# Performance work log

Measured on AMD Instinct MI355X. Metric: run time of the kernel, lower is better.

Reference implementation:

```python
import jax, jax.numpy as jnp
import numpy as np

B, S, D = 2, 2048, 1024
H, KV, HD = 16, 4, 64          # heads, kv heads, head_dim = D//H
I, E, K = 3584, 4, 2            # ffn intermediate, routed experts, top_k
WIN = 512                       # sliding window
EPS = 1e-5
THETA = 1000000.0
LIMIT = 7.0                     # swiglu clamp
NREP = H // KV
NEG = -1e30

def _rms(x, w):
    return x * jax.lax.rsqrt(jnp.mean(x * x, axis=-1, keepdims=True) + EPS) * w

def _rot_half(x):
    h = x.shape[-1] // 2
    return jnp.concatenate([-x[..., h:], x[..., :h]], axis=-1)

def _ffn(x, gw, uw, dw):
    g = jnp.minimum(x @ gw.T, LIMIT)
    u = jnp.clip(x @ uw.T, -LIMIT, LIMIT)
    return (jax.nn.silu(g) * u) @ dw.T

def setup_inputs():
    key = jax.random.key(0)
    ks = jax.random.split(key, 16)
    # rotary embeddings [S, HD]
    inv = 1.0 / (THETA ** (jnp.arange(0, HD, 2, dtype=jnp.float32) / HD))
    freqs = jnp.outer(jnp.arange(S, dtype=jnp.float32), inv)
    emb = jnp.concatenate([freqs, freqs], axis=-1)
    s = 0.02
    return dict(
        x=jax.random.normal(ks[0], (B, S, D), jnp.float32),
        cos=jnp.cos(emb), sin=jnp.sin(emb),
        attn_norm_w=jnp.ones((D,), jnp.float32),
        post_norm_w=jnp.ones((D,), jnp.float32),
        q_norm_w=jnp.ones((HD,), jnp.float32),
        k_norm_w=jnp.ones((HD,), jnp.float32),
        wq=jax.random.normal(ks[1], (H * HD, D), jnp.float32) * s,
        wk=jax.random.normal(ks[2], (KV * HD, D), jnp.float32) * s,
        wv=jax.random.normal(ks[3], (KV * HD, D), jnp.float32) * s,
        wo=jax.random.normal(ks[4], (D, H * HD), jnp.float32) * s,
        sinks=jax.random.normal(ks[5], (H,), jnp.float32),
        gate_w=jax.random.normal(ks[6], (E, D), jnp.float32) * s,
        eg_w=jax.random.normal(ks[7], (E, I, D), jnp.float32) * s,
        eu_w=jax.random.normal(ks[8], (E, I, D), jnp.float32) * s,
        ed_w=jax.random.normal(ks[9], (E, D, I), jnp.float32) * s,
        sg_w=jax.random.normal(ks[10], (I, D), jnp.float32) * s,
        su_w=jax.random.normal(ks[11], (I, D), jnp.float32) * s,
        sd_w=jax.random.normal(ks[12], (D, I), jnp.float32) * s,
    )

def _forward(x, cos, sin, attn_norm_w, wq, wk, wv, wo, q_norm_w, k_norm_w,
             sinks, post_norm_w, gate_w, eg_w, eu_w, ed_w, sg_w, su_w, sd_w):
    # ---- attention sublayer ----
    hin = _rms(x, attn_norm_w)
    q = (hin @ wq.T).reshape(B, S, H, HD)
    k = (hin @ wk.T).reshape(B, S, KV, HD)
    v = (hin @ wv.T).reshape(B, S, KV, HD)
    q = _rms(q, q_norm_w)
    k = _rms(k, k_norm_w)
    c, sn = cos[None, :, None, :], sin[None, :, None, :]
    q = q * c + _rot_half(q) * sn
    k = k * c + _rot_half(k) * sn
    k = jnp.repeat(k, NREP, axis=2)  # GQA -> [B,S,H,HD]
    v = jnp.repeat(v, NREP, axis=2)
    scores = jnp.einsum('bihd,bjhd->bhij', q, k) / np.sqrt(HD).astype(np.float32)
    idx = jnp.arange(S)
    allowed = (idx[:, None] >= idx[None, :]) & (idx[None, :] > idx[:, None] - WIN)
    scores = jnp.where(allowed[None, None], scores, NEG)
    sink = jnp.broadcast_to(sinks.reshape(1, H, 1, 1), (B, H, S, 1))
    ext = jnp.concatenate([scores, sink], axis=-1)           # [B,H,S,S+1]
    w = jax.nn.softmax(ext.astype(jnp.float32), axis=-1)[..., :-1].astype(x.dtype)
    attn = jnp.einsum('bhij,bjhd->bihd', w, v).reshape(B, S, H * HD) @ wo.T
    h1 = x + attn
    # ---- MoE FFN sublayer ----
    m = _rms(h1, post_norm_w).reshape(-1, D)                 # [T,D]
    T = m.shape[0]
    gs = jax.nn.softmax(m @ gate_w.T, axis=-1)               # [T,E]
    tw, ti = jax.lax.top_k(gs, K)
    tw = tw / (jnp.sum(tw, axis=-1, keepdims=True) + 1e-20)  # norm_topk_prob
    wd = jnp.zeros((T, E), m.dtype).at[jnp.arange(T)[:, None], ti].add(tw)
    g = jnp.minimum(jnp.einsum('td,eid->tei', m, eg_w), LIMIT)
    u = jnp.clip(jnp.einsum('td,eid->tei', m, eu_w), -LIMIT, LIMIT)
    eo = jnp.einsum('tei,edi->ted', jax.nn.silu(g) * u, ed_w)
    y = jnp.einsum('ted,te->td', eo, wd) + _ffn(m, sg_w, su_w, sd_w)
    return h1 + y.reshape(B, S, D)

def reference(x, cos, sin, attn_norm_w, post_norm_w, q_norm_w, k_norm_w,
              wq, wk, wv, wo, sinks, gate_w, eg_w, eu_w, ed_w, sg_w, su_w, sd_w):
    return _forward(x, cos, sin, attn_norm_w, wq, wk, wv, wo, q_norm_w, k_norm_w,
                    sinks, post_norm_w, gate_w, eg_w, eu_w, ed_w, sg_w, su_w, sd_w)
```

## Files before the change

### kernel.cpp

```cpp
#include <hip/hip_runtime.h>
#include <cstdint>
#include <cstddef>

#define S_LEN 2048
#define BATCH 2
#define DMODEL 1024
#define NH 16
#define NKV 4
#define HDIM 64
#define NTOK 4096
#define IDIM 3584
#define NEXP 4
#define WINSZ 512
#define EPSV 1e-5f
#define LIMV 7.0f
#define CATMAX 13056

typedef unsigned short u16;
typedef unsigned int u32;
typedef __bf16 bf16x8 __attribute__((ext_vector_type(8)));
typedef float f32x4 __attribute__((ext_vector_type(4)));
typedef u32 u32x4 __attribute__((ext_vector_type(4)));
typedef u16 u16x4 __attribute__((ext_vector_type(4)));

__device__ __forceinline__ u16 f2b(float f) {
  union { float f; u32 u; } v; v.f = f;
  return (u16)((v.u + 0x7fffu + ((v.u >> 16) & 1u)) >> 16);
}
__device__ __forceinline__ float b2f(u16 h) {
  union { u32 u; float f; } v; v.u = ((u32)h) << 16; return v.f;
}
__device__ __forceinline__ float wave_sum(float x) {
#pragma unroll
  for (int o = 32; o > 0; o >>= 1) x += __shfl_xor(x, o);
  return x;
}
__device__ __forceinline__ void gld16(const void* g, void* l) {
  __builtin_amdgcn_global_load_lds(
      (const __attribute__((address_space(1))) u32*)g,
      (__attribute__((address_space(3))) u32*)l, 16, 0, 0);
}

__global__ void k_init(int* cnt) {
  if (threadIdx.x < NEXP) cnt[threadIdx.x] = 0;
}

struct CvtArgs {
  const float* src[10];
  u16* dh[10];
  u16* dl[10];
  int n4[10];
};
__global__ __launch_bounds__(256) void k_convert(CvtArgs a) {
  int ai = blockIdx.y;
  const f32x4* s = (const f32x4*)a.src[ai];
  u16* dh = a.dh[ai];
  u16* dl = a.dl[ai];
  int n4 = a.n4[ai];
  for (int i = blockIdx.x * 256 + threadIdx.x; i < n4; i += gridDim.x * 256) {
    f32x4 v = s[i];
    u16x4 h;
    h.x = f2b(v.x); h.y = f2b(v.y); h.z = f2b(v.z); h.w = f2b(v.w);
    ((u16x4*)dh)[i] = h;
    if (dl) {
      u16x4 lo;
      lo.x = f2b(v.x - b2f(h.x)); lo.y = f2b(v.y - b2f(h.y));
      lo.z = f2b(v.z - b2f(h.z)); lo.w = f2b(v.w - b2f(h.w));
      ((u16x4*)dl)[i] = lo;
    }
  }
}

__global__ __launch_bounds__(256) void k_rms_split(const float* __restrict__ x,
                                                   const float* __restrict__ w,
                                                   u16* __restrict__ oh, u16* __restrict__ ol) {
  int row = blockIdx.x;
  int t = threadIdx.x;
  const f32x4* xr = (const f32x4*)(x + (size_t)row * DMODEL);
  f32x4 v = xr[t];
  float ss = v.x * v.x + v.y * v.y + v.z * v.z + v.w * v.w;
  ss = wave_sum(ss);
  __shared__ float red[4];
  int wid = t >> 6;
  if ((t & 63) == 0) red[wid] = ss;
  __syncthreads();
  float tot = red[0] + red[1] + red[2] + red[3];
  float r = rsqrtf(tot * (1.0f / DMODEL) + EPSV);
  f32x4 wv = ((const f32x4*)w)[t];
  float y0 = v.x * r * wv.x, y1 = v.y * r * wv.y, y2 = v.z * r * wv.z, y3 = v.w * r * wv.w;
  u16x4 h; h.x = f2b(y0); h.y = f2b(y1); h.z = f2b(y2); h.w = f2b(y3);
  u16x4 lo; lo.x = f2b(y0 - b2f(h.x)); lo.y = f2b(y1 - b2f(h.y));
  lo.z = f2b(y2 - b2f(h.z)); lo.w = f2b(y3 - b2f(h.w));
  ((u16x4*)(oh + (size_t)row * DMODEL))[t] = h;
  ((u16x4*)(ol + (size_t)row * DMODEL))[t] = lo;
}

__global__ __launch_bounds__(256) void k_qkprep(const float* __restrict__ qkv,
                                                const float* __restrict__ cosb,
                                                const float* __restrict__ sinb,
                                                const float* __restrict__ qw,
                                                const float* __restrict__ kw,
                                                u16* __restrict__ qhh, u16* __restrict__ qll,
                                                u16* __restrict__ khh, u16* __restrict__ kll,
                                                u16* __restrict__ vhh, u16* __restrict__ vll) {
  int t = blockIdx.x;
  int b = t / S_LEN, s = t - b * S_LEN;
  int wid = threadIdx.x >> 6, l = threadIdx.x & 63;
  const float* row = qkv + (size_t)t * 1536;
  float c = cosb[s * 64 + l], sn = sinb[s * 64 + l];
#pragma unroll
  for (int ii = 0; ii < 6; ii++) {
    int u = wid + 4 * ii;
    if (u < 16) {
      float v = row[u * 64 + l];
      float ss = wave_sum(v * v);
      float r = rsqrtf(ss * (1.0f / 64.0f) + EPSV);
      float vn = v * r * qw[l];
      float p = __shfl_xor(vn, 32);
      float o = (l < 32) ? (vn * c - p * sn) : (vn * c + p * sn);
      o *= 0.125f;
      size_t base = (((size_t)(b * NH + u)) * S_LEN + s) * 64 + l;
      u16 hi = f2b(o);
      qhh[base] = hi; qll[base] = f2b(o - b2f(hi));
    } else if (u < 20) {
      int kv = u - 16;
      float v = row[1024 + kv * 64 + l];
      float ss = wave_sum(v * v);
      float r = rsqrtf(ss * (1.0f / 64.0f) + EPSV);
      float vn = v * r * kw[l];
      float p = __shfl_xor(vn, 32);
      float o = (l < 32) ? (vn * c - p * sn) : (vn * c + p * sn);
      size_t base = (((size_t)(b * NKV + kv)) * S_LEN + s) * 64 + l;
      u16 hi = f2b(o);
      khh[base] = hi; kll[base] = f2b(o - b2f(hi));
    } else {
      int kv = u - 20;
      float v = row[1280 + kv * 64 + l];
      size_t base = (((size_t)(b * NKV + kv)) * S_LEN + s) * 64 + l;
      u16 hi = f2b(v);
      vhh[base] = hi; vll[base] = f2b(v - b2f(hi));
    }
  }
}

__global__ __launch_bounds__(256) void k_vtrans(const u16* __restrict__ vh,
                                                const u16* __restrict__ vl,
                                                u16* __restrict__ vth, u16* __restrict__ vtl) {
  int kb = blockIdx.x;
  int gg = blockIdx.y;
  __shared__ u16 Th[128 * 64], Tl[128 * 64];
  int t = threadIdx.x;
  const u16* sh = vh + (((size_t)gg * S_LEN) + kb * 128) * 64;
  const u16* sl = vl + (((size_t)gg * S_LEN) + kb * 128) * 64;
#pragma unroll
  for (int p = 0; p < 8; p++) {
    int idx = p * 256 + t;
    int key = idx >> 4, dq = idx & 15;
    u16x4 a = *(const u16x4*)(sh + key * 64 + dq * 4);
    u16x4 bb = *(const u16x4*)(sl + key * 64 + dq * 4);
    int off = key * 128 + ((dq * 8) ^ ((key & 7) << 4));
    *(u16x4*)((char*)Th + off) = a;
    *(u16x4*)((char*)Tl + off) = bb;
  }
  __syncthreads();
  int d = t >> 2, kq = t & 3;
  u16 outh[32], outl[32];
#pragma unroll
  for (int jj = 0; jj < 32; jj++) {
    int key = kq * 32 + jj;
    int off = key * 128 + ((d * 2) ^ ((key & 7) << 4));
    outh[jj] = *(const u16*)((const char*)Th + off);
    outl[jj] = *(const u16*)((const char*)Tl + off);
  }
  u16* dsth = vth + (((size_t)gg * 64) + d) * S_LEN + kb * 128 + kq * 32;
  u16* dstl = vtl + (((size_t)gg * 64) + d) * S_LEN + kb * 128 + kq * 32;
#pragma unroll
  for (int q4 = 0; q4 < 8; q4++) {
    u16x4 a = {outh[q4 * 4], outh[q4 * 4 + 1], outh[q4 * 4 + 2], outh[q4 * 4 + 3]};
    u16x4 bb = {outl[q4 * 4], outl[q4 * 4 + 1], outl[q4 * 4 + 2], outl[q4 * 4 + 3]};
    *(u16x4*)(dsth + q4 * 4) = a;
    *(u16x4*)(dstl + q4 * 4) = bb;
  }
}

__global__ __launch_bounds__(256) void k_attn_mfma(
    const u16* __restrict__ qhp, const u16* __restrict__ qlp,
    const u16* __restrict__ khp, const u16* __restrict__ klp,
    const u16* __restrict__ vthp, const u16* __restrict__ vtlp,
    const float* __restrict__ sinks,
    u16* __restrict__ oh, u16* __restrict__ ol) {
  int qt = blockIdx.x;
  int bh = blockIdx.y;
  int h = bh & 15, b = bh >> 4;
  int kvg = b * NKV + (h >> 2);
  int qbase = qt * 64;
  int t = threadIdx.x, w = t >> 6, l = t & 63;
  int g = l >> 4, li = l & 15;

  __shared__ u16 Qh[4096], Ql[4096], Kh[4096], Kl[4096], Vh[4096], Vl[4096];
  __shared__ u16 Ph[4][1024], Pl[4][1024];

  {
    const u16* sh = qhp + (((size_t)bh * S_LEN) + qbase) * 64;
    const u16* sl = qlp + (((size_t)bh * S_LEN) + qbase) * 64;
#pragma unroll
    for (int p = 0; p < 2; p++) {
      int idx = p * 256 + t;
      int row = idx >> 3, seg = idx & 7;
      u32x4 a = *(const u32x4*)(sh + row * 64 + seg * 8);
      u32x4 bb = *(const u32x4*)(sl + row * 64 + seg * 8);
      int off = row * 128 + ((seg * 16) ^ ((row & 7) << 4));
      *(u32x4*)((char*)Qh + off) = a;
      *(u32x4*)((char*)Ql + off) = bb;
    }
  }

  float m_[4], lsum[4];
  f32x4 accv[4];
  float sk = sinks[h];
#pragma unroll
  for (int j = 0; j < 4; j++) { m_[j] = sk; lsum[j] = 1.0f; }
#pragma unroll
  for (int nt = 0; nt < 4; nt++) accv[nt] = (f32x4){0.f, 0.f, 0.f, 0.f};

  int j0s = qbase - WINSZ; if (j0s < 0) j0s = 0;
  const u16* khb = khp + ((size_t)kvg * S_LEN) * 64;
  const u16* klb = klp + ((size_t)kvg * S_LEN) * 64;
  const u16* vthb = vthp + ((size_t)kvg * 64) * S_LEN;
  const u16* vtlb = vtlp + ((size_t)kvg * 64) * S_LEN;

  for (int j0 = j0s; j0 <= qbase; j0 += 64) {
    __syncthreads();
#pragma unroll
    for (int p = 0; p < 2; p++) {
      int idx = p * 256 + t;
      int row = idx >> 3, seg = idx & 7;
      int off = row * 128 + ((seg * 16) ^ ((row & 7) << 4));
      *(u32x4*)((char*)Kh + off) = *(const u32x4*)(khb + ((size_t)(j0 + row)) * 64 + seg * 8);
      *(u32x4*)((char*)Kl + off) = *(const u32x4*)(klb + ((size_t)(j0 + row)) * 64 + seg * 8);
      *(u32x4*)((char*)Vh + off) = *(const u32x4*)(vthb + (size_t)row * S_LEN + j0 + seg * 8);
      *(u32x4*)((char*)Vl + off) = *(const u32x4*)(vtlb + (size_t)row * S_LEN + j0 + seg * 8);
    }
    __syncthreads();

    f32x4 S[4];
#pragma unroll
    for (int nt = 0; nt < 4; nt++) S[nt] = (f32x4){0.f, 0.f, 0.f, 0.f};
#pragma unroll
    for (int ks = 0; ks < 2; ks++) {
      int arow = w * 16 + li;
      int coff = ks * 64 + g * 16;
      int ao = arow * 128 + (coff ^ ((arow & 7) << 4));
      bf16x8 qah = *(const bf16x8*)((char*)Qh + ao);
      bf16x8 qal = *(const bf16x8*)((char*)Ql + ao);
#pragma unroll
      for (int nt = 0; nt < 4; nt++) {
        int brow = nt * 16 + li;
        int bo = brow * 128 + (coff ^ ((brow & 7) << 4));
        bf16x8 kbh = *(const bf16x8*)((char*)Kh + bo);
        bf16x8 kbl = *(const bf16x8*)((char*)Kl + bo);
        S[nt] = __builtin_amdgcn_mfma_f32_16x16x32_bf16(qah, kbh, S[nt], 0, 0, 0);
        S[nt] = __builtin_amdgcn_mfma_f32_16x16x32_bf16(qah, kbl, S[nt], 0, 0, 0);
        S[nt] = __builtin_amdgcn_mfma_f32_16x16x32_bf16(qal, kbh, S[nt], 0, 0, 0);
      }
    }

    float scj[4];
#pragma unroll
    for (int j = 0; j < 4; j++) {
      int q = qbase + w * 16 + g * 4 + j;
      float sv[4];
      float mx = -1e30f;
#pragma unroll
      for (int nt = 0; nt < 4; nt++) {
        int key = j0 + nt * 16 + li;
        bool ok = (key <= q) && (key > q - WINSZ);
        sv[nt] = ok ? S[nt][j] : -1e30f;
        mx = fmaxf(mx, sv[nt]);
      }
#pragma unroll
      for (int o = 1; o < 16; o <<= 1) mx = fmaxf(mx, __shfl_xor(mx, o));
      float mn = fmaxf(m_[j], mx);
      float sc = __expf(m_[j] - mn);
      float ps = 0.f;
      float pv[4];
#pragma unroll
      for (int nt = 0; nt < 4; nt++) { pv[nt] = __expf(sv[nt] - mn); ps += pv[nt]; }
#pragma unroll
      for (int o = 1; o < 16; o <<= 1) ps += __shfl_xor(ps, o);
      lsum[j] = lsum[j] * sc + ps;
      m_[j] = mn;
      scj[j] = sc;
      int prow = g * 4 + j;
#pragma unroll
      for (int nt = 0; nt < 4; nt++) {
        int pb = prow * 128 + ((nt * 32 + li * 2) ^ ((prow & 7) << 4));
        u16 hi = f2b(pv[nt]);
        *(u16*)((char*)Ph[w] + pb) = hi;
        *(u16*)((char*)Pl[w] + pb) = f2b(pv[nt] - b2f(hi));
      }
    }
#pragma unroll
    for (int nt = 0; nt < 4; nt++) {
      f32x4 a = accv[nt];
      a[0] *= scj[0]; a[1] *= scj[1]; a[2] *= scj[2]; a[3] *= scj[3];
      accv[nt] = a;
    }

#pragma unroll
    for (int ks = 0; ks < 2; ks++) {
      int coff = ks * 64 + g * 16;
      int pb = li * 128 + (coff ^ ((li & 7) << 4));
      bf16x8 pah = *(const bf16x8*)((char*)Ph[w] + pb);
      bf16x8 pal = *(const bf16x8*)((char*)Pl[w] + pb);
#pragma unroll
      for (int nt = 0; nt < 4; nt++) {
        int vrow = nt * 16 + li;
        int vo = vrow * 128 + (coff ^ ((vrow & 7) << 4));
        bf16x8 vbh = *(const bf16x8*)((char*)Vh + vo);
        bf16x8 vbl = *(const bf16x8*)((char*)Vl + vo);
        accv[nt] = __builtin_amdgcn_mfma_f32_16x16x32_bf16(pah, vbh, accv[nt], 0, 0, 0);
        accv[nt] = __builtin_amdgcn_mfma_f32_16x16x32_bf16(pah, vbl, accv[nt], 0, 0, 0);
        accv[nt] = __builtin_amdgcn_mfma_f32_16x16x32_bf16(pal, vbh, accv[nt], 0, 0, 0);
      }
    }
  }

  float inv[4];
#pragma unroll
  for (int j = 0; j < 4; j++) inv[j] = 1.0f / lsum[j];
#pragma unroll
  for (int nt = 0; nt < 4; nt++) {
#pragma unroll
    for (int j = 0; j < 4; j++) {
      float o = accv[nt][j] * inv[j];
      int token = b * S_LEN + qbase + w * 16 + g * 4 + j;
      size_t off = (size_t)token * (NH * HDIM) + h * 64 + nt * 16 + li;
      u16 hi = f2b(o);
      oh[off] = hi;
      ol[off] = f2b(o - b2f(hi));
    }
  }
}

__global__ __launch_bounds__(256) void k_routing1(const float* __restrict__ h1,
                                                  const float* __restrict__ pw,
                                                  const float* __restrict__ gw,
                                                  u16* __restrict__ mb,
                                                  float* __restrict__ lgbuf) {
  int row = blockIdx.x;
  int t = threadIdx.x;
  int wid = t >> 6;
  const f32x4* xr = (const f32x4*)(h1 + (size_t)row * DMODEL);
  f32x4 v = xr[t];
  float ss = wave_sum(v.x * v.x + v.y * v.y + v.z * v.z + v.w * v.w);
  __shared__ float red[4];
  __shared__ float redp[4][4];
  if ((t & 63) == 0) red[wid] = ss;
  __syncthreads();
  float tot = red[0] + red[1] + red[2] + red[3];
  float r = rsqrtf(tot * (1.0f / DMODEL) + EPSV);
  f32x4 w4 = ((const f32x4*)pw)[t];
  float m0 = v.x * r * w4.x, m1 = v.y * r * w4.y, m2 = v.z * r * w4.z, m3 = v.w * r * w4.w;
  u16x4 hb; hb.x = f2b(m0); hb.y = f2b(m1); hb.z = f2b(m2); hb.w = f2b(m3);
  ((u16x4*)(mb + (size_t)row * DMODEL))[t] = hb;
#pragma unroll
  for (int e = 0; e < NEXP; e++) {
    f32x4 g4 = ((const f32x4*)(gw + (size_t)e * DMODEL))[t];
    float pe = wave_sum(m0 * g4.x + m1 * g4.y + m2 * g4.z + m3 * g4.w);
    if ((t & 63) == 0) redp[wid][e] = pe;
  }
  __syncthreads();
  if (t < NEXP) {
    float lg = redp[0][t] + redp[1][t] + redp[2][t] + redp[3][t];
    lgbuf[(size_t)row * NEXP + t] = lg;
  }
}

__global__ __launch_bounds__(256) void k_route2(const float* __restrict__ lgbuf,
                                                float* __restrict__ wd,
                                                int* __restrict__ cnt,
                                                int* __restrict__ idxb) {
  __shared__ int lcnt[NEXP], gbase[NEXP];
  int t = threadIdx.x;
  int token = blockIdx.x * 256 + t;
  if (t < NEXP) lcnt[t] = 0;
  __syncthreads();
  f32x4 lgv = ((const f32x4*)lgbuf)[token];
  float lg[4] = {lgv.x, lgv.y, lgv.z, lgv.w};
  int i1 = 0;
#pragma unroll
  for (int e = 1; e < NEXP; e++) if (lg[e] > lg[i1]) i1 = e;
  int i2 = -1;
#pragma unroll
  for (int e = 0; e < NEXP; e++) if (e != i1 && (i2 < 0 || lg[e] > lg[i2])) i2 = e;
  float d = __expf(lg[i2] - lg[i1]);
  float w1 = 1.0f / (1.0f + d);
  float w2 = 1.0f - w1;
  float wrow[4] = {0.f, 0.f, 0.f, 0.f};
  wrow[i1] = w1; wrow[i2] = w2;
  ((f32x4*)wd)[token] = (f32x4){wrow[0], wrow[1], wrow[2], wrow[3]};
  int r1 = atomicAdd(&lcnt[i1], 1);
  int r2 = atomicAdd(&lcnt[i2], 1);
  __syncthreads();
  if (t < NEXP) gbase[t] = atomicAdd(&cnt[t], lcnt[t]);
  __syncthreads();
  idxb[i1 * NTOK + gbase[i1] + r1] = token * 2;
  idxb[i2 * NTOK + gbase[i2] + r2] = token * 2 + 1;
}

__global__ __launch_bounds__(256) void k_route3(const int* __restrict__ cnt,
                                                const int* __restrict__ idxb,
                                                const float* __restrict__ wd,
                                                int* __restrict__ idxcat,
                                                float* __restrict__ wcat,
                                                int* __restrict__ pref) {
  int i = blockIdx.x * 256 + threadIdx.x;
  int c0 = cnt[0], c1 = cnt[1], c2 = cnt[2], c3 = cnt[3];
  int p1 = (c0 + 255) & ~255;
  int p2 = p1 + ((c1 + 255) & ~255);
  int p3 = p2 + ((c2 + 255) & ~255);
  int p4 = p3 + ((c3 + 255) & ~255);
  int p5 = p4 + NTOK;
  if (i == 0) {
    pref[0] = 0; pref[1] = p1; pref[2] = p2; pref[3] = p3; pref[4] = p4; pref[5] = p5;
  }
  if (i >= CATMAX) return;
  if (i >= p5) { idxcat[i] = -1; wcat[i] = 0.f; return; }
  if (i >= p4) {
    idxcat[i] = (i - p4) * 4 + 2;
    wcat[i] = 1.0f;
    return;
  }
  int e, base, cn;
  if (i < p1) { e = 0; base = 0; cn = c0; }
  else if (i < p2) { e = 1; base = p1; cn = c1; }
  else if (i < p3) { e = 2; base = p2; cn = c2; }
  else { e = 3; base = p3; cn = c3; }
  int j = i - base;
  if (j < cn) {
    int entry = idxb[e * NTOK + j];
    idxcat[i] = (entry >> 1) * 4 + (entry & 1);
    wcat[i] = wd[(size_t)(entry >> 1) * NEXP + e];
  } else {
    idxcat[i] = -1;
    wcat[i] = 0.f;
  }
}

template <bool DUAL>
__global__ __launch_bounds__(512, 1) void k256(
    const u16* __restrict__ A, const u16* __restrict__ B1e,
    const u16* __restrict__ B2e,
    int lda, int ldb, int K,
    const int* __restrict__ idxcat, const float* __restrict__ wcat,
    const int* __restrict__ pref,
    u16* __restrict__ actout, u16* __restrict__ y3) {
  __shared__ u16 As[4][256 * 32];
  __shared__ u16 B1s[4][128 * 32];
  __shared__ u16 B2s[4][DUAL ? 128 * 32 : 1];
  int tm = blockIdx.y, tn = blockIdx.x;
  int Meff = pref[5];
  int r0 = tm * 256;
  if (r0 >= Meff) return;
  int e = (r0 < pref[1]) ? 0 : (r0 < pref[2]) ? 1 : (r0 < pref[3]) ? 2
          : (r0 < pref[4]) ? 3 : 4;
  const u16* B1 = B1e + (size_t)e * IDIM * DMODEL;
  const u16* B2 = DUAL ? (B2e + (size_t)e * IDIM * DMODEL) : nullptr;

  int t = threadIdx.x;
  int w = t >> 6, l = t & 63;
  int wm = w >> 2, wn = w & 3;
  int li = l & 15, lh = l >> 4;

  size_t aG[2];
#pragma unroll
  for (int c = 0; c < 2; c++) {
    int g = c * 512 + t;
    int rowi = g >> 2, seg = g & 3;
    int srcc = (seg - (rowi >> 2)) & 3;
    int row;
    if constexpr (DUAL) {
      int en = idxcat[r0 + rowi];
      row = (en >= 0) ? (en >> 2) : 0;
    } else {
      row = r0 + rowi;
    }
    aG[c] = (size_t)row * lda + srcc * 8;
  }
  size_t bG;
  {
    int rowi = t >> 2, seg = t & 3;
    int srcc = (seg - (rowi >> 2)) & 3;
    bG = (size_t)(tn * 128 + rowi) * ldb + srcc * 8;
  }
  int wlds = w * 1024;

  int sread = (lh + (li >> 2)) & 3;
  int abase = (wm * 128 + li) * 64 + sread * 16;
  int bbase = (wn * 32 + li) * 64 + sread * 16;

  f32x4 acc[8][2];
  f32x4 accU[DUAL ? 8 : 1][2];
#pragma unroll
  for (int f = 0; f < 8; f++)
#pragma unroll
    for (int cf = 0; cf < 2; cf++) {
      acc[f][cf] = (f32x4){0.f, 0.f, 0.f, 0.f};
      if constexpr (DUAL) accU[f][cf] = (f32x4){0.f, 0.f, 0.f, 0.f};
    }

  auto stage = [&](u16* as, u16* b1s, u16* b2s, int k0) {
    gld16(A + aG[0] + k0, (char*)as + wlds);
    gld16(A + aG[1] + k0, (char*)as + 8192 + wlds);
    gld16(B1 + bG + k0, (char*)b1s + wlds);
    if constexpr (DUAL) gld16(B2 + bG + k0, (char*)b2s + wlds);
  };

  int NT = K >> 5;
  stage(As[0], B1s[0], B2s[0], 0);
  stage(As[1], B1s[1], B2s[1], 32);
  stage(As[2], B1s[2], B2s[2], 64);

  auto iter = [&](int tt, u16* as, u16* b1s, u16* b2s,
                  u16* asN, u16* b1sN, u16* b2sN) {
    if (tt + 3 < NT) stage(asN, b1sN, b2sN, (tt + 3) << 5);
    __builtin_amdgcn_sched_barrier(0);
    if constexpr (DUAL) {
      asm volatile("s_waitcnt vmcnt(12)" ::: "memory");
    } else {
      asm volatile("s_waitcnt vmcnt(9)" ::: "memory");
    }
    __builtin_amdgcn_s_barrier();
    __builtin_amdgcn_sched_barrier(0);
    bf16x8 af[8];
#pragma unroll
    for (int f = 0; f < 8; f++)
      af[f] = *(const bf16x8*)((const char*)as + abase + f * 1024);
    bf16x8 b1f[2];
#pragma unroll
    for (int cf = 0; cf < 2; cf++)
      b1f[cf] = *(const bf16x8*)((const char*)b1s + bbase + cf * 1024);
#pragma unroll
    for (int f = 0; f < 8; f++)
#pragma unroll
      for (int cf = 0; cf < 2; cf++)
        acc[f][cf] = __builtin_amdgcn_mfma_f32_16x16x32_bf16(af[f], b1f[cf], acc[f][cf], 0, 0, 0);
    if constexpr (DUAL) {
      bf16x8 b2f[2];
#pragma unroll
      for (int cf = 0; cf < 2; cf++)
        b2f[cf] = *(const bf16x8*)((const char*)b2s + bbase + cf * 1024);
#pragma unroll
      for (int f = 0; f < 8; f++)
#pragma unroll
        for (int cf = 0; cf < 2; cf++)
          accU[f][cf] = __builtin_amdgcn_mfma_f32_16x16x32_bf16(af[f], b2f[cf], accU[f][cf], 0, 0, 0);
    }
    __builtin_amdgcn_s_barrier();
    __builtin_amdgcn_sched_barrier(0);
  };

  for (int kt = 0; kt < NT; kt += 4) {
    iter(kt + 0, As[0], B1s[0], B2s[0], As[3], B1s[3], B2s[3]);
    iter(kt + 1, As[1], B1s[1], B2s[1], As[0], B1s[0], B2s[0]);
    iter(kt + 2, As[2], B1s[2], B2s[2], As[1], B1s[1], B2s[1]);
    iter(kt + 3, As[3], B1s[3], B2s[3], As[2], B1s[2], B2s[2]);
  }

#pragma unroll
  for (int f = 0; f < 8; f++) {
#pragma unroll
    for (int j = 0; j < 4; j++) {
      int r = r0 + wm * 128 + f * 16 + lh * 4 + j;
#pragma unroll
      for (int cf = 0; cf < 2; cf++) {
        int c = tn * 128 + wn * 32 + cf * 16 + li;
        if constexpr (DUAL) {
          float g = acc[f][cf][j];
          float u = accU[f][cf][j];
          float gm = fminf(g, LIMV);
          float um = fminf(fmaxf(u, -LIMV), LIMV);
          float a = gm / (1.0f + __expf(-gm)) * um;
          actout[(size_t)r * IDIM + c] = f2b(a);
        } else {
          int entry = idxcat[r];
          if (entry >= 0) {
            int tok = entry >> 2, slot = entry & 3;
            y3[((size_t)slot * NTOK + tok) * DMODEL + c] = f2b(wcat[r] * acc[f][cf][j]);
          }
        }
      }
    }
  }
}

constexpr int EPI_STORE = 0;
constexpr int EPI_H1 = 1;

template <int EPI>
__global__ __launch_bounds__(256, 2) void k_gemm(
    const u16* __restrict__ Ah, const u16* __restrict__ Al,
    const u16* __restrict__ Bh, const u16* __restrict__ Bl,
    int M, int N, int K, int lda, int ldb,
    float* __restrict__ outF, int ldc, int col0,
    const float* __restrict__ addsrc) {
  __shared__ u16 As[2 * 128 * 32];
  __shared__ u16 Bs[2 * 128 * 32];
  int tm = blockIdx.y, tn = blockIdx.x;
  int t = threadIdx.x;
  int w = t >> 6, l = t & 63;
  int wr = w >> 1, wc = w & 1;

  size_t a0 = (size_t)(tm * 128 + (t >> 2)) * lda + (t & 3) * 8;
  size_t a1 = a0 + (size_t)64 * lda;
  size_t b0 = (size_t)(tn * 128 + (t >> 2)) * ldb + (t & 3) * 8;
  size_t b1 = b0 + (size_t)64 * ldb;

  char* AsW0 = (char*)As + w * 1024;
  char* AsW1 = (char*)As + 4096 + w * 1024;
  char* BsW0 = (char*)Bs + w * 1024;
  char* BsW1 = (char*)Bs + 4096 + w * 1024;

  f32x4 acc[4][4];
#pragma unroll
  for (int i = 0; i < 4; i++)
#pragma unroll
    for (int j = 0; j < 4; j++) acc[i][j] = (f32x4){0.f, 0.f, 0.f, 0.f};

  int arow = wr * 64 + (l & 15);
  int brow = wc * 64 + (l & 15);
  int koff = (l >> 4) * 8;

  for (int k0 = 0; k0 < K; k0 += 32) {
    __syncthreads();
    gld16(Ah + a0 + k0, AsW0);
    gld16(Ah + a1 + k0, AsW1);
    gld16(Bh + b0 + k0, BsW0);
    gld16(Bh + b1 + k0, BsW1);
    gld16(Al + a0 + k0, AsW0 + 8192);
    gld16(Al + a1 + k0, AsW1 + 8192);
    gld16(Bl + b0 + k0, BsW0 + 8192);
    gld16(Bl + b1 + k0, BsW1 + 8192);
    __syncthreads();
    bf16x8 af[2][4], bf[2][4];
#pragma unroll
    for (int mm = 0; mm < 4; mm++) {
      af[0][mm] = *(const bf16x8*)&As[(arow + mm * 16) * 32 + koff];
      bf[0][mm] = *(const bf16x8*)&Bs[(brow + mm * 16) * 32 + koff];
      af[1][mm] = *(const bf16x8*)&As[128 * 32 + (arow + mm * 16) * 32 + koff];
      bf[1][mm] = *(const bf16x8*)&Bs[128 * 32 + (brow + mm * 16) * 32 + koff];
    }
#pragma unroll
    for (int mi = 0; mi < 4; mi++)
#pragma unroll
      for (int ni = 0; ni < 4; ni++) {
        acc[mi][ni] = __builtin_amdgcn_mfma_f32_16x16x32_bf16(af[0][mi], bf[0][ni], acc[mi][ni], 0, 0, 0);
        acc[mi][ni] = __builtin_amdgcn_mfma_f32_16x16x32_bf16(af[0][mi], bf[1][ni], acc[mi][ni], 0, 0, 0);
        acc[mi][ni] = __builtin_amdgcn_mfma_f32_16x16x32_bf16(af[1][mi], bf[0][ni], acc[mi][ni], 0, 0, 0);
      }
  }

  int rb = tm * 128 + wr * 64 + ((l >> 4) << 2);
  int cb = tn * 128 + wc * 64 + (l & 15);
#pragma unroll
  for (int mi = 0; mi < 4; mi++) {
#pragma unroll
    for (int j = 0; j < 4; j++) {
      int r = rb + mi * 16 + j;
#pragma unroll
      for (int ni = 0; ni < 4; ni++) {
        int c = cb + ni * 16;
        float v = acc[mi][ni][j];
        if constexpr (EPI == EPI_STORE) {
          outF[(size_t)r * ldc + col0 + c] = v;
        } else {
          size_t o = (size_t)r * ldc + c;
          outF[o] = v + addsrc[o];
        }
      }
    }
  }
}

__global__ __launch_bounds__(256) void k_final(const float* __restrict__ h1,
                                               const u16* __restrict__ y3,
                                               float* __restrict__ out) {
  int i = blockIdx.x * 256 + threadIdx.x;
  f32x4 a = ((const f32x4*)h1)[i];
  u16x4 s0 = ((const u16x4*)y3)[i];
  u16x4 s1 = ((const u16x4*)(y3 + (size_t)NTOK * DMODEL))[i];
  u16x4 s2 = ((const u16x4*)(y3 + (size_t)2 * NTOK * DMODEL))[i];
  f32x4 r = {a.x + b2f(s0.x) + b2f(s1.x) + b2f(s2.x),
             a.y + b2f(s0.y) + b2f(s1.y) + b2f(s2.y),
             a.z + b2f(s0.z) + b2f(s1.z) + b2f(s2.z),
             a.w + b2f(s0.w) + b2f(s1.w) + b2f(s2.w)};
  ((f32x4*)out)[i] = r;
}

extern "C" void kernel_launch(void* const* d_in, const int* in_sizes, int n_in,
                              void* d_out, int out_size, void* d_ws, size_t ws_size,
                              hipStream_t stream) {
  (void)in_sizes; (void)n_in; (void)out_size; (void)ws_size;
  const float* x = (const float*)d_in[0];
  const float* cosb = (const float*)d_in[1];
  const float* sinb = (const float*)d_in[2];
  const float* anw = (const float*)d_in[3];
  const float* pnw = (const float*)d_in[4];
  const float* qnw = (const float*)d_in[5];
  const float* knw = (const float*)d_in[6];
  const float* wq = (const float*)d_in[7];
  const float* wk = (const float*)d_in[8];
  const float* wv = (const float*)d_in[9];
  const float* wo = (const float*)d_in[10];
  const float* sinks = (const float*)d_in[11];
  const float* gw = (const float*)d_in[12];
  const float* egw = (const float*)d_in[13];
  const float* euw = (const float*)d_in[14];
  const float* edw = (const float*)d_in[15];
  const float* sgw = (const float*)d_in[16];
  const float* suw = (const float*)d_in[17];
  const float* sdw = (const float*)d_in[18];
  float* out = (float*)d_out;

  char* ws = (char*)d_ws;
  size_t off = 0;
  auto alloc = [&](size_t bytes) -> char* {
    char* p = ws + off;
    off += (bytes + 255) & ~(size_t)255;
    return p;
  };
  const size_t EW = (size_t)IDIM * DMODEL;
  u16* wqkvh = (u16*)alloc((size_t)1536 * 1024 * 2);
  u16* wqkvl = (u16*)alloc((size_t)1536 * 1024 * 2);
  u16* woh = (u16*)alloc(1048576 * 2); u16* wol = (u16*)alloc(1048576 * 2);
  u16* egb5 = (u16*)alloc(5 * EW * 2);
  u16* eub5 = (u16*)alloc(5 * EW * 2);
  u16* edb5 = (u16*)alloc(5 * EW * 2);
  float* h1 = (float*)alloc((size_t)NTOK * DMODEL * 4);
  u16* mb = (u16*)alloc((size_t)NTOK * DMODEL * 2);
  u16* y3 = (u16*)alloc((size_t)3 * NTOK * DMODEL * 2);
  float* wdbuf = (float*)alloc((size_t)NTOK * NEXP * 4);
  float* lgbuf = (float*)alloc((size_t)NTOK * NEXP * 4);
  int* cnt = (int*)alloc(256);
  int* idxb = (int*)alloc((size_t)NEXP * NTOK * 4);
  int* idxcat = (int*)alloc((size_t)CATMAX * 4);
  float* wcat = (float*)alloc((size_t)CATMAX * 4);
  int* pref = (int*)alloc(256);
  char* regA = alloc((size_t)CATMAX * IDIM * 2);
  float* qkvb = (float*)regA;
  u16* qh_ = (u16*)(regA + 25165824);
  u16* ql_ = (u16*)(regA + 33554432);
  u16* kh_ = (u16*)(regA + 41943040);
  u16* kl_ = (u16*)(regA + 44040192);
  u16* vh_ = (u16*)(regA + 46137344);
  u16* vl_ = (u16*)(regA + 48234496);
  u16* vth_ = (u16*)(regA + 50331648);
  u16* vtl_ = (u16*)(regA + 52428800);
  u16* hinh = (u16*)(regA + 54525952);
  u16* hinl = (u16*)(regA + 62914560);
  u16* attnh = (u16*)(regA + 71303168);
  u16* attnl = (u16*)(regA + 79691776);
  u16* actcat = (u16*)regA;

  k_init<<<1, 64, 0, stream>>>(cnt);

  CvtArgs ca;
  const float* srcs[10] = {wq, wk, wv, wo, egw, euw, edw, sgw, suw, sdw};
  u16* dhs[10] = {wqkvh, wqkvh + 1048576, wqkvh + 1310720, woh,
                  egb5, eub5, edb5, egb5 + 4 * EW, eub5 + 4 * EW, edb5 + 4 * EW};
  u16* dls[10] = {wqkvl, wqkvl + 1048576, wqkvl + 1310720, wol,
                  nullptr, nullptr, nullptr, nullptr, nullptr, nullptr};
  int ns[10] = {1048576, 262144, 262144, 1048576, 14680064, 14680064, 14680064,
                3670016, 3670016, 3670016};
  for (int i = 0; i < 10; i++) {
    ca.src[i] = srcs[i]; ca.dh[i] = dhs[i]; ca.dl[i] = dls[i]; ca.n4[i] = ns[i] / 4;
  }
  k_convert<<<dim3(2048, 10), 256, 0, stream>>>(ca);

  k_rms_split<<<NTOK, 256, 0, stream>>>(x, anw, hinh, hinl);

  k_gemm<EPI_STORE><<<dim3(12, 32), 256, 0, stream>>>(
      hinh, hinl, wqkvh, wqkvl, NTOK, 1536, 1024, 1024, 1024,
      qkvb, 1536, 0, nullptr);

  k_qkprep<<<NTOK, 256, 0, stream>>>(qkvb, cosb, sinb, qnw, knw,
                                     qh_, ql_, kh_, kl_, vh_, vl_);
  k_vtrans<<<dim3(16, 8), 256, 0, stream>>>(vh_, vl_, vth_, vtl_);
  k_attn_mfma<<<dim3(32, 32), 256, 0, stream>>>(qh_, ql_, kh_, kl_, vth_, vtl_,
                                                sinks, attnh, attnl);

  k_gemm<EPI_H1><<<dim3(8, 32), 256, 0, stream>>>(
      attnh, attnl, woh, wol, NTOK, 1024, 1024, 1024, 1024,
      h1, 1024, 0, x);

  k_routing1<<<NTOK, 256, 0, stream>>>(h1, pnw, gw, mb, lgbuf);
  k_route2<<<16, 256, 0, stream>>>(lgbuf, wdbuf, cnt, idxb);
  k_route3<<<CATMAX / 256, 256, 0, stream>>>(cnt, idxb, wdbuf, idxcat, wcat, pref);

  k256<true><<<dim3(IDIM / 128, CATMAX / 256), 512, 0, stream>>>(
      mb, egb5, eub5, DMODEL, DMODEL, DMODEL, idxcat, wcat, pref, actcat, nullptr);
  k256<false><<<dim3(DMODEL / 128, CATMAX / 256), 512, 0, stream>>>(
      actcat, edb5, nullptr, IDIM, IDIM, IDIM, idxcat, wcat, pref, nullptr, y3);

  k_final<<<4096, 256, 0, stream>>>(h1, y3, out);
}
```

Baseline: 721.1 us.

## Re-layout MoE GEMM shared-memory tiles with XOR swizzle and raise occupancy

Reorganises how the MoE expert GEMM kernel stages A/B tiles into shared memory: each LDS row now holds two 32-wide K-chunks halves with an XOR swizzle, and the fragment read addresses change to match. It also sets launch bounds to allow two blocks per CU, issues a dummy stage on the final iterations so the vmcnt wait counts stay uniform, hoists the B2 fragment loads before the MFMAs, and raises wave priority around the MFMA block. The aim is fewer LDS bank conflicts and better latency hiding. The register cap from 2 blocks/CU risks spills given the large accumulator arrays, and the dummy loads add extra memory traffic at the tail.

```diff
diff --git a/kernel.cpp b/kernel.cpp
--- a/kernel.cpp
+++ b/kernel.cpp
@@ -449,7 +449,7 @@
 }
 
 template <bool DUAL>
-__global__ __launch_bounds__(512, 1) void k256(
+__global__ __launch_bounds__(512, 2) void k256(
     const u16* __restrict__ A, const u16* __restrict__ B1e,
     const u16* __restrict__ B2e,
     int lda, int ldb, int K,
@@ -473,32 +473,30 @@
   int wm = w >> 2, wn = w & 3;
   int li = l & 15, lh = l >> 4;
 
+  int g = (l & 7) ^ (l >> 3);
+  int kchunk = g & 3;
   size_t aG[2];
 #pragma unroll
   for (int c = 0; c < 2; c++) {
-    int g = c * 512 + t;
-    int rowi = g >> 2, seg = g & 3;
-    int srcc = (seg - (rowi >> 2)) & 3;
+    int rA = c * 64 + w * 8 + (l >> 3) + 128 * (g >> 2);
     int row;
     if constexpr (DUAL) {
-      int en = idxcat[r0 + rowi];
+      int en = idxcat[r0 + rA];
       row = (en >= 0) ? (en >> 2) : 0;
     } else {
-      row = r0 + rowi;
-    }
-    aG[c] = (size_t)row * lda + srcc * 8;
+      row = r0 + rA;
+    }
+    aG[c] = (size_t)row * lda + kchunk * 8;
   }
   size_t bG;
   {
-    int rowi = t >> 2, seg = t & 3;
-    int srcc = (seg - (rowi >> 2)) & 3;
-    bG = (size_t)(tn * 128 + rowi) * ldb + srcc * 8;
+    int rB = w * 8 + (l >> 3) + 64 * (g >> 2);
+    bG = (size_t)(tn * 128 + rB) * ldb + kchunk * 8;
   }
   int wlds = w * 1024;
 
-  int sread = (lh + (li >> 2)) & 3;
-  int abase = (wm * 128 + li) * 64 + sread * 16;
-  int bbase = (wn * 32 + li) * 64 + sread * 16;
+  int abase = li * 128 + (((wm * 4 + lh) ^ (li & 7)) << 4);
+  int bbase = ((wn & 1) * 32 + li) * 128 + ((((wn >> 1) * 4 + lh) ^ (li & 7)) << 4);
 
   f32x4 acc[8][2];
   f32x4 accU[DUAL ? 8 : 1][2];
@@ -522,9 +520,10 @@
   stage(As[1], B1s[1], B2s[1], 32);
   stage(As[2], B1s[2], B2s[2], 64);
 
-  auto iter = [&](int tt, u16* as, u16* b1s, u16* b2s,
+  auto iter = [&](int tt, const u16* as, const u16* b1s, const u16* b2s,
                   u16* asN, u16* b1sN, u16* b2sN) {
-    if (tt + 3 < NT) stage(asN, b1sN, b2sN, (tt + 3) << 5);
+    int kn = (tt + 3 < NT) ? ((tt + 3) << 5) : 0;
+    stage(asN, b1sN, b2sN, kn);
     __builtin_amdgcn_sched_barrier(0);
     if constexpr (DUAL) {
       asm volatile("s_waitcnt vmcnt(12)" ::: "memory");
@@ -536,27 +535,31 @@
     bf16x8 af[8];
 #pragma unroll
     for (int f = 0; f < 8; f++)
-      af[f] = *(const bf16x8*)((const char*)as + abase + f * 1024);
+      af[f] = *(const bf16x8*)((const char*)as + abase + f * 2048);
     bf16x8 b1f[2];
 #pragma unroll
     for (int cf = 0; cf < 2; cf++)
-      b1f[cf] = *(const bf16x8*)((const char*)b1s + bbase + cf * 1024);
+      b1f[cf] = *(const bf16x8*)((const char*)b1s + bbase + cf * 2048);
+    bf16x8 b2f[2];
+    if constexpr (DUAL) {
+#pragma unroll
+      for (int cf = 0; cf < 2; cf++)
+        b2f[cf] = *(const bf16x8*)((const char*)b2s + bbase + cf * 2048);
+    }
+    __builtin_amdgcn_s_setprio(1);
 #pragma unroll
     for (int f = 0; f < 8; f++)
 #pragma unroll
       for (int cf = 0; cf < 2; cf++)
         acc[f][cf] = __builtin_amdgcn_mfma_f32_16x16x32_bf16(af[f], b1f[cf], acc[f][cf], 0, 0, 0);
     if constexpr (DUAL) {
-      bf16x8 b2f[2];
-#pragma unroll
-      for (int cf = 0; cf < 2; cf++)
-        b2f[cf] = *(const bf16x8*)((const char*)b2s + bbase + cf * 1024);
 #pragma unroll
       for (int f = 0; f < 8; f++)
 #pragma unroll
         for (int cf = 0; cf < 2; cf++)
           accU[f][cf] = __builtin_amdgcn_mfma_f32_16x16x32_bf16(af[f], b2f[cf], accU[f][cf], 0, 0, 0);
     }
+    __builtin_amdgcn_s_setprio(0);
     __builtin_amdgcn_s_barrier();
     __builtin_amdgcn_sched_barrier(0);
   };
@@ -577,9 +580,9 @@
       for (int cf = 0; cf < 2; cf++) {
         int c = tn * 128 + wn * 32 + cf * 16 + li;
         if constexpr (DUAL) {
-          float g = acc[f][cf][j];
+          float gv = acc[f][cf][j];
           float u = accU[f][cf][j];
-          float gm = fminf(g, LIMV);
+          float gm = fminf(gv, LIMV);
           float um = fminf(fmaxf(u, -LIMV), LIMV);
           float a = gm / (1.0f + __expf(-gm)) * um;
           actout[(size_t)r * IDIM + c] = f2b(a);
```

Measured after the change: 704.5 us. -2.3%, faster.
